# Kernel tuning notes

Measured on AMD Instinct MI355X. Metric: run time of the kernel, lower is better.

The kernel has to match this reference:

```python
import jax, jax.numpy as jnp
import numpy as np

B, H, W, C = 8, 64, 64, 128
BN_EPS = 1e-3  # keras BatchNormalization default epsilon


def setup_inputs() -> dict:
    key = jax.random.key(0)
    ks = jax.random.split(key, 8)
    scale = 1.0 / np.sqrt(C)
    return {
        "x": jax.random.normal(ks[0], (B, H, W, C), dtype=jnp.float32),
        "wq": jax.random.normal(ks[1], (C, C), dtype=jnp.float32) * scale,
        "bq": jnp.zeros((C,), dtype=jnp.float32),
        "wk": jax.random.normal(ks[2], (C, C), dtype=jnp.float32) * scale,
        "bk": jnp.zeros((C,), dtype=jnp.float32),
        "wv": jax.random.normal(ks[3], (C, C), dtype=jnp.float32) * scale,
        "bv": jnp.zeros((C,), dtype=jnp.float32),
        "gamma": jnp.ones((C,), dtype=jnp.float32),
        "beta": jnp.zeros((C,), dtype=jnp.float32),
        "mov_mean": jax.random.normal(ks[4], (C,), dtype=jnp.float32) * 0.1,
        "mov_var": jax.random.uniform(ks[5], (C,), dtype=jnp.float32) * 0.5 + 0.5,
    }


def reference(x, wq, bq, wk, bk, wv, bv, gamma, beta, mov_mean, mov_var):
    b, h, w, c = x.shape
    n = h * w
    # 1x1 convs == per-pixel linear projections
    q = (jnp.einsum('bhwc,cd->bhwd', x, wq) + bq).reshape(b, n, c)
    k = (jnp.einsum('bhwc,cd->bhwd', x, wk) + bk).reshape(b, n, c)
    v = (jnp.einsum('bhwc,cd->bhwd', x, wv) + bv).reshape(b, n, c)
    # full [n, n] attention matrix (as in the original module)
    scores = jnp.einsum('bnc,bmc->bnm', q, k) / jnp.sqrt(jnp.asarray(c, x.dtype))
    attn = jax.nn.softmax(scores, axis=-1)  # dropout is identity in inference
    out = jnp.einsum('bnm,bmc->bnc', attn, v).reshape(b, h, w, c)
    out = out + x  # residual
    # BatchNormalization, inference mode (moving statistics)
    inv = gamma * jax.lax.rsqrt(mov_var + BN_EPS)
    out = out * inv + (beta - mov_mean * inv)
    return out
```

## Files before the change

kernel.cpp:

```cpp
#include <hip/hip_runtime.h>


typedef __attribute__((ext_vector_type(8))) short bf16x8;
typedef __attribute__((ext_vector_type(4))) float f32x4;

__device__ __forceinline__ unsigned short f2bf(float f) {
  unsigned int u = __builtin_bit_cast(unsigned int, f);
  u += 0x7fffu + ((u >> 16) & 1u);
  return (unsigned short)(u >> 16);
}
__device__ __forceinline__ unsigned int pack2(float a, float b) {
  return (unsigned int)f2bf(a) | ((unsigned int)f2bf(b) << 16);
}
__device__ __forceinline__ unsigned int pack2t(float a, float b) {
  return __builtin_amdgcn_perm(__builtin_bit_cast(unsigned int, b),
                               __builtin_bit_cast(unsigned int, a),
                               0x07060302u);
}
__device__ __forceinline__ float fexp2(float x) {
  return __builtin_amdgcn_exp2f(x);
}

__device__ __forceinline__ void dma16(const void* g, void* l) {
  __builtin_amdgcn_global_load_lds(
      (const __attribute__((address_space(1))) unsigned int*)g,
      (__attribute__((address_space(3))) unsigned int*)l, 16, 0, 0);
}

#define SCALE_Q (0.08838834764831845f * 1.44269504088896340f)

__global__ __launch_bounds__(256) void prep_wt(
    const float* __restrict__ wq, const float* __restrict__ wk,
    const float* __restrict__ wv, unsigned short* __restrict__ wt) {
  __shared__ float ws[128 * 129];
  const float* W = (blockIdx.x == 0) ? wq : (blockIdx.x == 1 ? wk : wv);
  const float sc = (blockIdx.x == 0) ? SCALE_Q : 1.0f;
  unsigned short* out = wt + blockIdx.x * 16384;
  const int t = threadIdx.x;

#pragma unroll
  for (int i = 0; i < 16; ++i) {
    int e = (i * 256 + t) * 4;
    float4 v = *(const float4*)(W + e);
    int k = e >> 7, c = e & 127;
    float* d = ws + k * 129 + c;
    d[0] = v.x; d[1] = v.y; d[2] = v.z; d[3] = v.w;
  }
  __syncthreads();

  const int c = t & 15, n0 = t >> 4;
#pragma unroll
  for (int pass = 0; pass < 8; ++pass) {
    int n = pass * 16 + n0;
    const float* col = ws + n;
    unsigned int u0 = pack2(col[(c * 8 + 0) * 129] * sc, col[(c * 8 + 1) * 129] * sc);
    unsigned int u1 = pack2(col[(c * 8 + 2) * 129] * sc, col[(c * 8 + 3) * 129] * sc);
    unsigned int u2 = pack2(col[(c * 8 + 4) * 129] * sc, col[(c * 8 + 5) * 129] * sc);
    unsigned int u3 = pack2(col[(c * 8 + 6) * 129] * sc, col[(c * 8 + 7) * 129] * sc);
    *(uint4*)(out + n * 128 + c * 8) = make_uint4(u0, u1, u2, u3);
  }
}

__global__ __launch_bounds__(256) void qkv_proj(
    const float* __restrict__ x, const unsigned short* __restrict__ wt,
    const float* __restrict__ bq, const float* __restrict__ bk, const float* __restrict__ bv,
    unsigned short* __restrict__ Qg, unsigned short* __restrict__ Kg,
    unsigned short* __restrict__ Vtg) {
  __shared__ unsigned short xs[64 * 128];
  __shared__ unsigned short obuf[9216];
  const int t = threadIdx.x;
  const int rowblk = blockIdx.x * 64;

#pragma unroll
  for (int i = 0; i < 8; ++i) {
    int flat = t * 4 + i * 1024;
    int row = flat >> 7, col = flat & 127;
    float4 v = *(const float4*)(x + (size_t)(rowblk + row) * 128 + col);
    unsigned int u0 = pack2(v.x, v.y), u1 = pack2(v.z, v.w);
    int pos = (col >> 3) ^ (row & 15);
    *(uint2*)(xs + row * 128 + pos * 8 + (col & 7)) = make_uint2(u0, u1);
  }
  __syncthreads();

  const int lane = t & 63, wv_ = t >> 6;
  const int lm = lane & 15, quad = lane >> 4;

  bf16x8 a[4];
  {
    int row = wv_ * 16 + lm;
#pragma unroll
    for (int ks = 0; ks < 4; ++ks)
      a[ks] = __builtin_bit_cast(bf16x8,
          *(const uint4*)(xs + row * 128 + (((ks * 4 + quad) ^ lm) * 8)));
  }

  const int b   = rowblk >> 12;
  const int nb0 = rowblk & 4095;
  const f32x4 zero4 = {0.f, 0.f, 0.f, 0.f};

#pragma unroll
  for (int p = 0; p < 3; ++p) {
    const unsigned short* w = wt + p * 16384;
    const float* bias = (p == 0) ? bq : (p == 1 ? bk : bv);
    const float bsc = (p == 0) ? SCALE_Q : 1.0f;

    f32x4 acc[8];
#pragma unroll
    for (int ct = 0; ct < 8; ++ct) acc[ct] = zero4;

#pragma unroll
    for (int ct = 0; ct < 8; ++ct) {
      int n = ct * 16 + lm;
      const uint4* wp = (const uint4*)(w + n * 128 + quad * 8);
#pragma unroll
      for (int ks = 0; ks < 4; ++ks) {
        bf16x8 bfr = __builtin_bit_cast(bf16x8, wp[ks * 4]);
        acc[ct] = __builtin_amdgcn_mfma_f32_16x16x32_bf16(a[ks], bfr, acc[ct], 0, 0, 0);
      }
    }

    if (p < 2) {
      int rowb = wv_ * 16 + quad * 4;
#pragma unroll
      for (int ct = 0; ct < 8; ++ct) {
        int c = ct * 16 + lm;
        float bb = bias[c] * bsc;
#pragma unroll
        for (int r = 0; r < 4; ++r)
          obuf[(rowb + r) * 136 + c] = f2bf(acc[ct][r] + bb);
      }
      __syncthreads();
      unsigned short* og = (p == 0) ? Qg : Kg;
      int row = t >> 2;
#pragma unroll
      for (int j = 0; j < 4; ++j) {
        int pos = (t & 3) * 4 + j;
        int ch  = (p == 1) ? (pos ^ (row & 15)) : pos;
        uint4 vv = *(const uint4*)(obuf + row * 136 + ch * 8);
        *(uint4*)(og + (size_t)(rowblk + row) * 128 + pos * 8) = vv;
      }
      __syncthreads();
    } else {
      int key_base = wv_ * 16 + quad * 4;
#pragma unroll
      for (int ct = 0; ct < 8; ++ct) {
        int c = ct * 16 + lm;
        float bb = bias[c];
        unsigned int u0 = pack2(acc[ct][0] + bb, acc[ct][1] + bb);
        unsigned int u1 = pack2(acc[ct][2] + bb, acc[ct][3] + bb);
        *(uint2*)(obuf + c * 72 + key_base) = make_uint2(u0, u1);
      }
      __syncthreads();
      int d = t >> 1;
#pragma unroll
      for (int j = 0; j < 4; ++j) {
        int ch = (t & 1) * 4 + j;
        uint4 vv = *(const uint4*)(obuf + d * 72 + ch * 8);
        *(uint4*)(Vtg + (size_t)b * 524288 + (size_t)d * 4096 + nb0 + ch * 8) = vv;
      }
    }
  }
}

__global__ __launch_bounds__(256)
__attribute__((amdgpu_waves_per_eu(2, 2)))
void flash_attn(
    const unsigned short* __restrict__ Qg, const unsigned short* __restrict__ Kg,
    const unsigned short* __restrict__ Vtg, const float* __restrict__ x,
    const float* __restrict__ gamma, const float* __restrict__ beta,
    const float* __restrict__ mmean, const float* __restrict__ mvar,
    float* __restrict__ out) {
  __shared__ unsigned short Kt[16384];
  __shared__ unsigned short Pbuf[2][8192];

  const int b  = blockIdx.x & 7;
  const int qt = blockIdx.x >> 3;
  const int t = threadIdx.x;
  const int lane = t & 63;
  const int w = t >> 6;
  const int lm = lane & 15, quad = lane >> 4;
  const int q0 = qt * 64;

  const unsigned short* Qb = Qg  + (size_t)b * 524288;
  const unsigned short* Kb = Kg  + (size_t)b * 524288;
  const unsigned short* Vb = Vtg + (size_t)b * 524288;

  {
    const unsigned short* src = Kb + (size_t)w * 4096 + lane * 8;
    unsigned short* dst = &Kt[w * 4096];
#pragma unroll
    for (int j = 0; j < 8; ++j) dma16(src + j * 512, dst + j * 512);
  }

  bf16x8 qf[4][4];
#pragma unroll
  for (int nt = 0; nt < 4; ++nt) {
    const uint4* qp = (const uint4*)(Qb + (size_t)(q0 + nt * 16 + lm) * 128 + quad * 8);
#pragma unroll
    for (int ks = 0; ks < 4; ++ks) qf[nt][ks] = __builtin_bit_cast(bf16x8, qp[ks * 4]);
  }

  const f32x4 zero4 = {0.f, 0.f, 0.f, 0.f};
  f32x4 o[2][4];
#pragma unroll
  for (int mt = 0; mt < 2; ++mt)
#pragma unroll
    for (int nt = 0; nt < 4; ++nt) o[mt][nt] = zero4;
  float lp[4] = {0.f, 0.f, 0.f, 0.f};
  bf16x8 vf[2][4];

#pragma unroll 1
  for (int kt = 0; kt < 32; ++kt) {
    const int key0 = kt * 128;

    asm volatile("s_waitcnt vmcnt(8)" ::: "memory");

    f32x4 sa[2][4];
#pragma unroll
    for (int mt = 0; mt < 2; ++mt)
#pragma unroll
      for (int nt = 0; nt < 4; ++nt) sa[mt][nt] = zero4;
#pragma unroll
    for (int mt = 0; mt < 2; ++mt) {
      const unsigned short* kr = &Kt[(w * 32 + mt * 16 + lm) * 128];
      bf16x8 kf[4];
#pragma unroll
      for (int ks = 0; ks < 4; ++ks)
        kf[ks] = __builtin_bit_cast(bf16x8, *(const uint4*)(kr + ((ks * 4 + quad) ^ lm) * 8));
#pragma unroll
      for (int ks = 0; ks < 4; ++ks)
#pragma unroll
        for (int nt = 0; nt < 4; ++nt)
          sa[mt][nt] = __builtin_amdgcn_mfma_f32_16x16x32_bf16(kf[ks], qf[nt][ks], sa[mt][nt], 0, 0, 0);
    }

    asm volatile("s_waitcnt lgkmcnt(0)" ::: "memory");
    if (kt + 1 < 32) {
      const unsigned short* src = Kb + (size_t)(kt + 1) * 16384 + w * 4096 + lane * 8;
      unsigned short* dst = &Kt[w * 4096];
#pragma unroll
      for (int j = 0; j < 8; ++j) dma16(src + j * 512, dst + j * 512);
    }

    if (kt > 0) {
      const uint4* Pr = (const uint4*)Pbuf[(kt & 1) ^ 1];
#pragma unroll
      for (int nt = 0; nt < 4; ++nt) {
        bf16x8 pf[4];
#pragma unroll
        for (int ks = 0; ks < 4; ++ks)
          pf[ks] = __builtin_bit_cast(bf16x8, Pr[(nt * 16 + lm) * 16 + ((ks * 4 + quad) ^ lm)]);
#pragma unroll
        for (int ks = 0; ks < 4; ++ks)
#pragma unroll
          for (int mt = 0; mt < 2; ++mt)
            o[mt][nt] = __builtin_amdgcn_mfma_f32_16x16x32_bf16(vf[mt][ks], pf[ks], o[mt][nt], 0, 0, 0);
      }
    }

#pragma unroll
    for (int mt = 0; mt < 2; ++mt) {
      const uint4* vp = (const uint4*)(Vb + (size_t)(w * 32 + mt * 16 + lm) * 4096 + key0 + quad * 8);
#pragma unroll
      for (int ks = 0; ks < 4; ++ks) vf[mt][ks] = __builtin_bit_cast(bf16x8, vp[ks * 4]);
    }

    {
      unsigned short* Ps = Pbuf[kt & 1];
      const int sub = (quad & 1) * 4;
#pragma unroll
      for (int mt = 0; mt < 2; ++mt) {
        int c16 = w * 4 + mt * 2 + (quad >> 1);
        int pos = c16 ^ lm;
#pragma unroll
        for (int nt = 0; nt < 4; ++nt) {
          float e0 = fexp2(sa[mt][nt][0]), e1 = fexp2(sa[mt][nt][1]);
          float e2 = fexp2(sa[mt][nt][2]), e3 = fexp2(sa[mt][nt][3]);
          lp[nt] += (e0 + e1) + (e2 + e3);
          *(uint2*)(Ps + (nt * 16 + lm) * 128 + pos * 8 + sub) =
              make_uint2(pack2t(e0, e1), pack2t(e2, e3));
        }
      }
    }

    asm volatile("s_waitcnt lgkmcnt(0)\n\ts_barrier" ::: "memory");
  }

  {
    const uint4* Pr = (const uint4*)Pbuf[1];
#pragma unroll
    for (int nt = 0; nt < 4; ++nt) {
      bf16x8 pf[4];
#pragma unroll
      for (int ks = 0; ks < 4; ++ks)
        pf[ks] = __builtin_bit_cast(bf16x8, Pr[(nt * 16 + lm) * 16 + ((ks * 4 + quad) ^ lm)]);
#pragma unroll
      for (int ks = 0; ks < 4; ++ks)
#pragma unroll
        for (int mt = 0; mt < 2; ++mt)
          o[mt][nt] = __builtin_amdgcn_mfma_f32_16x16x32_bf16(vf[mt][ks], pf[ks], o[mt][nt], 0, 0, 0);
    }
  }

  float* lred = (float*)Pbuf[0];
#pragma unroll
  for (int nt = 0; nt < 4; ++nt) {
    lp[nt] += __shfl_xor(lp[nt], 16);
    lp[nt] += __shfl_xor(lp[nt], 32);
  }
  if (quad == 0) {
#pragma unroll
    for (int nt = 0; nt < 4; ++nt) lred[w * 64 + nt * 16 + lm] = lp[nt];
  }
  __syncthreads();
  float rl[4];
#pragma unroll
  for (int nt = 0; nt < 4; ++nt) {
    int q = nt * 16 + lm;
    rl[nt] = 1.0f / ((lred[q] + lred[64 + q]) + (lred[128 + q] + lred[192 + q]));
  }

#pragma unroll
  for (int mt = 0; mt < 2; ++mt) {
    int c0 = w * 32 + mt * 16 + quad * 4;
    float4 gm = *(const float4*)(gamma + c0);
    float4 bt = *(const float4*)(beta + c0);
    float4 mm = *(const float4*)(mmean + c0);
    float4 mv = *(const float4*)(mvar + c0);
    float iv0 = gm.x * rsqrtf(mv.x + 1e-3f), iv1 = gm.y * rsqrtf(mv.y + 1e-3f);
    float iv2 = gm.z * rsqrtf(mv.z + 1e-3f), iv3 = gm.w * rsqrtf(mv.w + 1e-3f);
    float ad0 = bt.x - mm.x * iv0, ad1 = bt.y - mm.y * iv1;
    float ad2 = bt.z - mm.z * iv2, ad3 = bt.w - mm.w * iv3;
#pragma unroll
    for (int nt = 0; nt < 4; ++nt) {
      size_t g = ((size_t)b * 4096 + q0 + nt * 16 + lm) * 128 + c0;
      float4 xr = *(const float4*)(x + g);
      float4 ov;
      ov.x = (o[mt][nt][0] * rl[nt] + xr.x) * iv0 + ad0;
      ov.y = (o[mt][nt][1] * rl[nt] + xr.y) * iv1 + ad1;
      ov.z = (o[mt][nt][2] * rl[nt] + xr.z) * iv2 + ad2;
      ov.w = (o[mt][nt][3] * rl[nt] + xr.w) * iv3 + ad3;
      *(float4*)(out + g) = ov;
    }
  }
}

extern "C" void kernel_launch(void* const* d_in, const int* in_sizes, int n_in,
                              void* d_out, int out_size, void* d_ws, size_t ws_size,
                              hipStream_t stream) {
  const float* x     = (const float*)d_in[0];
  const float* wq    = (const float*)d_in[1];
  const float* bq    = (const float*)d_in[2];
  const float* wk    = (const float*)d_in[3];
  const float* bk    = (const float*)d_in[4];
  const float* wv    = (const float*)d_in[5];
  const float* bv    = (const float*)d_in[6];
  const float* gamma = (const float*)d_in[7];
  const float* beta  = (const float*)d_in[8];
  const float* mmean = (const float*)d_in[9];
  const float* mvar  = (const float*)d_in[10];
  float* out = (float*)d_out;

  unsigned short* wt  = (unsigned short*)d_ws;
  unsigned short* Qg  = wt + 3 * 128 * 128;
  unsigned short* Kg  = Qg + 8 * 4096 * 128;
  unsigned short* Vtg = Kg + 8 * 4096 * 128;

  prep_wt<<<dim3(3), dim3(256), 0, stream>>>(wq, wk, wv, wt);
  qkv_proj<<<dim3(512), dim3(256), 0, stream>>>(x, wt, bq, bk, bv, Qg, Kg, Vtg);
  flash_attn<<<dim3(512), dim3(256), 0, stream>>>(Qg, Kg, Vtg, x, gamma, beta,
                                                  mmean, mvar, out);
}
```

Baseline: 208.1 us.

## Split attention block across eight waves and drop P double-buffering

The attention kernel now launches 512 threads per block. Key/channel work is split across four wave groups and queries across two, so each wave holds half the query fragments and accumulators. The P double buffer and the one-iteration software pipeline (PV of the previous tile overlapped with QK of the current) are replaced by a single P buffer. This requires a second barrier per key tile, and V is now loaded at the top of each iteration. The aim is more waves per CU and lower register pressure to hide latency, at the cost of more synchronisation and less explicit overlap.

```diff
diff --git a/kernel.cpp b/kernel.cpp
--- a/kernel.cpp
+++ b/kernel.cpp
@@ -162,8 +162,8 @@
   }
 }
 
-__global__ __launch_bounds__(256)
-__attribute__((amdgpu_waves_per_eu(2, 2)))
+__global__ __launch_bounds__(512)
+__attribute__((amdgpu_waves_per_eu(4, 4)))
 void flash_attn(
     const unsigned short* __restrict__ Qg, const unsigned short* __restrict__ Kg,
     const unsigned short* __restrict__ Vtg, const float* __restrict__ x,
@@ -171,13 +171,14 @@
     const float* __restrict__ mmean, const float* __restrict__ mvar,
     float* __restrict__ out) {
   __shared__ unsigned short Kt[16384];
-  __shared__ unsigned short Pbuf[2][8192];
+  __shared__ unsigned short Pbuf[8192];
 
   const int b  = blockIdx.x & 7;
   const int qt = blockIdx.x >> 3;
   const int t = threadIdx.x;
   const int lane = t & 63;
   const int w = t >> 6;
+  const int kw = w >> 1, qw = w & 1;
   const int lm = lane & 15, quad = lane >> 4;
   const int q0 = qt * 64;
 
@@ -186,43 +187,51 @@
   const unsigned short* Vb = Vtg + (size_t)b * 524288;
 
   {
-    const unsigned short* src = Kb + (size_t)w * 4096 + lane * 8;
-    unsigned short* dst = &Kt[w * 4096];
-#pragma unroll
-    for (int j = 0; j < 8; ++j) dma16(src + j * 512, dst + j * 512);
-  }
-
-  bf16x8 qf[4][4];
-#pragma unroll
-  for (int nt = 0; nt < 4; ++nt) {
-    const uint4* qp = (const uint4*)(Qb + (size_t)(q0 + nt * 16 + lm) * 128 + quad * 8);
+    const unsigned short* src = Kb + (size_t)w * 2048 + lane * 8;
+    unsigned short* dst = &Kt[w * 2048];
+#pragma unroll
+    for (int j = 0; j < 4; ++j) dma16(src + j * 512, dst + j * 512);
+  }
+
+  bf16x8 qf[2][4];
+#pragma unroll
+  for (int nt = 0; nt < 2; ++nt) {
+    const uint4* qp = (const uint4*)(Qb + (size_t)(q0 + qw * 32 + nt * 16 + lm) * 128 + quad * 8);
 #pragma unroll
     for (int ks = 0; ks < 4; ++ks) qf[nt][ks] = __builtin_bit_cast(bf16x8, qp[ks * 4]);
   }
 
+  asm volatile("s_waitcnt vmcnt(8)" ::: "memory");
+  __builtin_amdgcn_s_barrier();
+
   const f32x4 zero4 = {0.f, 0.f, 0.f, 0.f};
-  f32x4 o[2][4];
+  f32x4 o[2][2];
 #pragma unroll
   for (int mt = 0; mt < 2; ++mt)
 #pragma unroll
-    for (int nt = 0; nt < 4; ++nt) o[mt][nt] = zero4;
-  float lp[4] = {0.f, 0.f, 0.f, 0.f};
-  bf16x8 vf[2][4];
+    for (int nt = 0; nt < 2; ++nt) o[mt][nt] = zero4;
+  float lp[2] = {0.f, 0.f};
 
 #pragma unroll 1
   for (int kt = 0; kt < 32; ++kt) {
     const int key0 = kt * 128;
 
-    asm volatile("s_waitcnt vmcnt(8)" ::: "memory");
-
-    f32x4 sa[2][4];
+    bf16x8 vf[2][4];
+#pragma unroll
+    for (int mt = 0; mt < 2; ++mt) {
+      const uint4* vp = (const uint4*)(Vb + (size_t)(kw * 32 + mt * 16 + lm) * 4096 + key0 + quad * 8);
+#pragma unroll
+      for (int ks = 0; ks < 4; ++ks) vf[mt][ks] = __builtin_bit_cast(bf16x8, vp[ks * 4]);
+    }
+
+    f32x4 sa[2][2];
 #pragma unroll
     for (int mt = 0; mt < 2; ++mt)
 #pragma unroll
-      for (int nt = 0; nt < 4; ++nt) sa[mt][nt] = zero4;
+      for (int nt = 0; nt < 2; ++nt) sa[mt][nt] = zero4;
 #pragma unroll
     for (int mt = 0; mt < 2; ++mt) {
-      const unsigned short* kr = &Kt[(w * 32 + mt * 16 + lm) * 128];
+      const unsigned short* kr = &Kt[(kw * 32 + mt * 16 + lm) * 128];
       bf16x8 kf[4];
 #pragma unroll
       for (int ks = 0; ks < 4; ++ks)
@@ -230,99 +239,77 @@
 #pragma unroll
       for (int ks = 0; ks < 4; ++ks)
 #pragma unroll
-        for (int nt = 0; nt < 4; ++nt)
+        for (int nt = 0; nt < 2; ++nt)
           sa[mt][nt] = __builtin_amdgcn_mfma_f32_16x16x32_bf16(kf[ks], qf[nt][ks], sa[mt][nt], 0, 0, 0);
     }
 
-    asm volatile("s_waitcnt lgkmcnt(0)" ::: "memory");
-    if (kt + 1 < 32) {
-      const unsigned short* src = Kb + (size_t)(kt + 1) * 16384 + w * 4096 + lane * 8;
-      unsigned short* dst = &Kt[w * 4096];
-#pragma unroll
-      for (int j = 0; j < 8; ++j) dma16(src + j * 512, dst + j * 512);
-    }
-
-    if (kt > 0) {
-      const uint4* Pr = (const uint4*)Pbuf[(kt & 1) ^ 1];
-#pragma unroll
-      for (int nt = 0; nt < 4; ++nt) {
-        bf16x8 pf[4];
-#pragma unroll
-        for (int ks = 0; ks < 4; ++ks)
-          pf[ks] = __builtin_bit_cast(bf16x8, Pr[(nt * 16 + lm) * 16 + ((ks * 4 + quad) ^ lm)]);
-#pragma unroll
-        for (int ks = 0; ks < 4; ++ks)
-#pragma unroll
-          for (int mt = 0; mt < 2; ++mt)
-            o[mt][nt] = __builtin_amdgcn_mfma_f32_16x16x32_bf16(vf[mt][ks], pf[ks], o[mt][nt], 0, 0, 0);
-      }
-    }
-
-#pragma unroll
-    for (int mt = 0; mt < 2; ++mt) {
-      const uint4* vp = (const uint4*)(Vb + (size_t)(w * 32 + mt * 16 + lm) * 4096 + key0 + quad * 8);
-#pragma unroll
-      for (int ks = 0; ks < 4; ++ks) vf[mt][ks] = __builtin_bit_cast(bf16x8, vp[ks * 4]);
-    }
-
     {
-      unsigned short* Ps = Pbuf[kt & 1];
       const int sub = (quad & 1) * 4;
 #pragma unroll
       for (int mt = 0; mt < 2; ++mt) {
-        int c16 = w * 4 + mt * 2 + (quad >> 1);
+        int c16 = kw * 4 + mt * 2 + (quad >> 1);
         int pos = c16 ^ lm;
 #pragma unroll
-        for (int nt = 0; nt < 4; ++nt) {
+        for (int nt = 0; nt < 2; ++nt) {
           float e0 = fexp2(sa[mt][nt][0]), e1 = fexp2(sa[mt][nt][1]);
           float e2 = fexp2(sa[mt][nt][2]), e3 = fexp2(sa[mt][nt][3]);
           lp[nt] += (e0 + e1) + (e2 + e3);
-          *(uint2*)(Ps + (nt * 16 + lm) * 128 + pos * 8 + sub) =
+          *(uint2*)(Pbuf + (qw * 32 + nt * 16 + lm) * 128 + pos * 8 + sub) =
               make_uint2(pack2t(e0, e1), pack2t(e2, e3));
         }
       }
     }
 
     asm volatile("s_waitcnt lgkmcnt(0)\n\ts_barrier" ::: "memory");
-  }
-
-  {
-    const uint4* Pr = (const uint4*)Pbuf[1];
-#pragma unroll
-    for (int nt = 0; nt < 4; ++nt) {
-      bf16x8 pf[4];
-#pragma unroll
-      for (int ks = 0; ks < 4; ++ks)
-        pf[ks] = __builtin_bit_cast(bf16x8, Pr[(nt * 16 + lm) * 16 + ((ks * 4 + quad) ^ lm)]);
-#pragma unroll
-      for (int ks = 0; ks < 4; ++ks)
-#pragma unroll
-        for (int mt = 0; mt < 2; ++mt)
-          o[mt][nt] = __builtin_amdgcn_mfma_f32_16x16x32_bf16(vf[mt][ks], pf[ks], o[mt][nt], 0, 0, 0);
-    }
-  }
-
-  float* lred = (float*)Pbuf[0];
-#pragma unroll
-  for (int nt = 0; nt < 4; ++nt) {
+
+    if (kt + 1 < 32) {
+      const unsigned short* src = Kb + (size_t)(kt + 1) * 16384 + w * 2048 + lane * 8;
+      unsigned short* dst = &Kt[w * 2048];
+#pragma unroll
+      for (int j = 0; j < 4; ++j) dma16(src + j * 512, dst + j * 512);
+    }
+
+    {
+      const uint4* Pr = (const uint4*)Pbuf;
+#pragma unroll
+      for (int nt = 0; nt < 2; ++nt) {
+        bf16x8 pf[4];
+#pragma unroll
+        for (int ks = 0; ks < 4; ++ks)
+          pf[ks] = __builtin_bit_cast(bf16x8, Pr[(qw * 32 + nt * 16 + lm) * 16 + ((ks * 4 + quad) ^ lm)]);
+#pragma unroll
+        for (int ks = 0; ks < 4; ++ks)
+#pragma unroll
+          for (int mt = 0; mt < 2; ++mt)
+            o[mt][nt] = __builtin_amdgcn_mfma_f32_16x16x32_bf16(vf[mt][ks], pf[ks], o[mt][nt], 0, 0, 0);
+      }
+    }
+
+    asm volatile("s_waitcnt vmcnt(0) lgkmcnt(0)\n\ts_barrier" ::: "memory");
+  }
+
+  float* lred = (float*)Pbuf;
+#pragma unroll
+  for (int nt = 0; nt < 2; ++nt) {
     lp[nt] += __shfl_xor(lp[nt], 16);
     lp[nt] += __shfl_xor(lp[nt], 32);
   }
   if (quad == 0) {
 #pragma unroll
-    for (int nt = 0; nt < 4; ++nt) lred[w * 64 + nt * 16 + lm] = lp[nt];
+    for (int nt = 0; nt < 2; ++nt)
+      lred[kw * 64 + qw * 32 + nt * 16 + lm] = lp[nt];
   }
   __syncthreads();
-  float rl[4];
-#pragma unroll
-  for (int nt = 0; nt < 4; ++nt) {
-    int q = nt * 16 + lm;
+  float rl[2];
+#pragma unroll
+  for (int nt = 0; nt < 2; ++nt) {
+    int q = qw * 32 + nt * 16 + lm;
     rl[nt] = 1.0f / ((lred[q] + lred[64 + q]) + (lred[128 + q] + lred[192 + q]));
   }
 
 #pragma unroll
   for (int mt = 0; mt < 2; ++mt) {
-    int c0 = w * 32 + mt * 16 + quad * 4;
+    int c0 = kw * 32 + mt * 16 + quad * 4;
     float4 gm = *(const float4*)(gamma + c0);
     float4 bt = *(const float4*)(beta + c0);
     float4 mm = *(const float4*)(mmean + c0);
@@ -332,8 +319,8 @@
     float ad0 = bt.x - mm.x * iv0, ad1 = bt.y - mm.y * iv1;
     float ad2 = bt.z - mm.z * iv2, ad3 = bt.w - mm.w * iv3;
 #pragma unroll
-    for (int nt = 0; nt < 4; ++nt) {
-      size_t g = ((size_t)b * 4096 + q0 + nt * 16 + lm) * 128 + c0;
+    for (int nt = 0; nt < 2; ++nt) {
+      size_t g = ((size_t)b * 4096 + q0 + qw * 32 + nt * 16 + lm) * 128 + c0;
       float4 xr = *(const float4*)(x + g);
       float4 ov;
       ov.x = (o[mt][nt][0] * rl[nt] + xr.x) * iv0 + ad0;
@@ -368,6 +355,6 @@
 
   prep_wt<<<dim3(3), dim3(256), 0, stream>>>(wq, wk, wv, wt);
   qkv_proj<<<dim3(512), dim3(256), 0, stream>>>(x, wt, bq, bk, bv, Qg, Kg, Vtg);
-  flash_attn<<<dim3(512), dim3(256), 0, stream>>>(Qg, Kg, Vtg, x, gamma, beta,
+  flash_attn<<<dim3(512), dim3(512), 0, stream>>>(Qg, Kg, Vtg, x, gamma, beta,
                                                   mmean, mvar, out);
 }
```

New measurement: 273.9 us. +31.6%, slower.

## Software-pipeline softmax exp of previous tile behind current QK MFMAs

Applied to the files above, without the earlier changes.

Restructures the flash attention key loop into a two-phase macro that keeps two score register sets. The exp/pack/store of the previous tile's scores is deferred so it can overlap with the current tile's QK^T MFMAs, and the PV product now follows a single barrier. The goal is to hide the exp and LDS write latency behind matrix work. The cost is an extra 32 accumulator registers, which risks spills under the two-waves-per-EU bound, plus a reworked epilogue for the last tile.

```diff
diff --git a/kernel.cpp b/kernel.cpp
--- a/kernel.cpp
+++ b/kernel.cpp
@@ -161,6 +161,75 @@
     }
   }
 }
+
+
+#define PHASE(KT, SAC, SAP)                                                    \
+  {                                                                            \
+    const int kt_ = (KT);                                                      \
+        \
+    asm volatile("s_waitcnt vmcnt(8)" ::: "memory");                           \
+    _Pragma("unroll") for (int mt = 0; mt < 2; ++mt)                           \
+      _Pragma("unroll") for (int nt = 0; nt < 4; ++nt) SAC[mt][nt] = zero4;    \
+    _Pragma("unroll") for (int mt = 0; mt < 2; ++mt) {                         \
+      const unsigned short* kr = &Kt[(w * 32 + mt * 16 + lm) * 128];           \
+      bf16x8 kf[4];                                                            \
+      _Pragma("unroll") for (int ks = 0; ks < 4; ++ks)                         \
+        kf[ks] = __builtin_bit_cast(                                           \
+            bf16x8, *(const uint4*)(kr + ((ks * 4 + quad) ^ lm) * 8));         \
+      _Pragma("unroll") for (int ks = 0; ks < 4; ++ks)                         \
+        _Pragma("unroll") for (int nt = 0; nt < 4; ++nt)                       \
+          SAC[mt][nt] = __builtin_amdgcn_mfma_f32_16x16x32_bf16(               \
+              kf[ks], qf[nt][ks], SAC[mt][nt], 0, 0, 0);                       \
+    }                                                                          \
+        \
+    if (kt_ > 0) {                                                             \
+      unsigned short* Ps = Pbuf[(kt_ - 1) & 1];                                \
+      const int sub = (quad & 1) * 4;                                          \
+      _Pragma("unroll") for (int mt = 0; mt < 2; ++mt) {                       \
+        int c16 = w * 4 + mt * 2 + (quad >> 1);                                \
+        int pos = c16 ^ lm;                                                    \
+        _Pragma("unroll") for (int nt = 0; nt < 4; ++nt) {                     \
+          float e0 = fexp2(SAP[mt][nt][0]), e1 = fexp2(SAP[mt][nt][1]);        \
+          float e2 = fexp2(SAP[mt][nt][2]), e3 = fexp2(SAP[mt][nt][3]);        \
+          lp[nt] += (e0 + e1) + (e2 + e3);                                     \
+          *(uint2*)(Ps + (nt * 16 + lm) * 128 + pos * 8 + sub) =               \
+              make_uint2(pack2t(e0, e1), pack2t(e2, e3));                      \
+        }                                                                      \
+      }                                                                        \
+    }                                                                          \
+       \
+    asm volatile("s_waitcnt lgkmcnt(0)" ::: "memory");                         \
+    if (kt_ + 1 < 32) {                                                        \
+      const unsigned short* src =                                              \
+          Kb + (size_t)(kt_ + 1) * 16384 + w * 4096 + lane * 8;                \
+      unsigned short* dst = &Kt[w * 4096];                                     \
+      _Pragma("unroll") for (int j = 0; j < 8; ++j)                            \
+        dma16(src + j * 512, dst + j * 512);                                   \
+    }                                                                          \
+              \
+    asm volatile("s_barrier" ::: "memory");                                    \
+                \
+    if (kt_ > 0) {                                                             \
+      const uint4* Pr = (const uint4*)Pbuf[(kt_ - 1) & 1];                     \
+      _Pragma("unroll") for (int nt = 0; nt < 4; ++nt) {                       \
+        bf16x8 pf[4];                                                          \
+        _Pragma("unroll") for (int ks = 0; ks < 4; ++ks)                       \
+          pf[ks] = __builtin_bit_cast(                                         \
+              bf16x8, Pr[(nt * 16 + lm) * 16 + ((ks * 4 + quad) ^ lm)]);       \
+        _Pragma("unroll") for (int ks = 0; ks < 4; ++ks)                       \
+          _Pragma("unroll") for (int mt = 0; mt < 2; ++mt)                     \
+            o[mt][nt] = __builtin_amdgcn_mfma_f32_16x16x32_bf16(               \
+                vf[mt][ks], pf[ks], o[mt][nt], 0, 0, 0);                       \
+      }                                                                        \
+    }                                                                          \
+                      \
+    _Pragma("unroll") for (int mt = 0; mt < 2; ++mt) {                         \
+      const uint4* vp = (const uint4*)(                                        \
+          Vb + (size_t)(w * 32 + mt * 16 + lm) * 4096 + kt_ * 128 + quad * 8); \
+      _Pragma("unroll") for (int ks = 0; ks < 4; ++ks)                         \
+        vf[mt][ks] = __builtin_bit_cast(bf16x8, vp[ks * 4]);                   \
+    }                                                                          \
+  }
 
 __global__ __launch_bounds__(256)
 __attribute__((amdgpu_waves_per_eu(2, 2)))
@@ -208,83 +277,32 @@
     for (int nt = 0; nt < 4; ++nt) o[mt][nt] = zero4;
   float lp[4] = {0.f, 0.f, 0.f, 0.f};
   bf16x8 vf[2][4];
+  f32x4 saA[2][4], saB[2][4];
 
 #pragma unroll 1
-  for (int kt = 0; kt < 32; ++kt) {
-    const int key0 = kt * 128;
-
-    asm volatile("s_waitcnt vmcnt(8)" ::: "memory");
-
-    f32x4 sa[2][4];
-#pragma unroll
-    for (int mt = 0; mt < 2; ++mt)
-#pragma unroll
-      for (int nt = 0; nt < 4; ++nt) sa[mt][nt] = zero4;
+  for (int kt2 = 0; kt2 < 16; ++kt2) {
+    PHASE(2 * kt2,     saA, saB)
+    PHASE(2 * kt2 + 1, saB, saA)
+  }
+
+  {
+    unsigned short* Ps = Pbuf[1];
+    const int sub = (quad & 1) * 4;
 #pragma unroll
     for (int mt = 0; mt < 2; ++mt) {
-      const unsigned short* kr = &Kt[(w * 32 + mt * 16 + lm) * 128];
-      bf16x8 kf[4];
-#pragma unroll
-      for (int ks = 0; ks < 4; ++ks)
-        kf[ks] = __builtin_bit_cast(bf16x8, *(const uint4*)(kr + ((ks * 4 + quad) ^ lm) * 8));
-#pragma unroll
-      for (int ks = 0; ks < 4; ++ks)
-#pragma unroll
-        for (int nt = 0; nt < 4; ++nt)
-          sa[mt][nt] = __builtin_amdgcn_mfma_f32_16x16x32_bf16(kf[ks], qf[nt][ks], sa[mt][nt], 0, 0, 0);
-    }
-
-    asm volatile("s_waitcnt lgkmcnt(0)" ::: "memory");
-    if (kt + 1 < 32) {
-      const unsigned short* src = Kb + (size_t)(kt + 1) * 16384 + w * 4096 + lane * 8;
-      unsigned short* dst = &Kt[w * 4096];
-#pragma unroll
-      for (int j = 0; j < 8; ++j) dma16(src + j * 512, dst + j * 512);
-    }
-
-    if (kt > 0) {
-      const uint4* Pr = (const uint4*)Pbuf[(kt & 1) ^ 1];
+      int c16 = w * 4 + mt * 2 + (quad >> 1);
+      int pos = c16 ^ lm;
 #pragma unroll
       for (int nt = 0; nt < 4; ++nt) {
-        bf16x8 pf[4];
-#pragma unroll
-        for (int ks = 0; ks < 4; ++ks)
-          pf[ks] = __builtin_bit_cast(bf16x8, Pr[(nt * 16 + lm) * 16 + ((ks * 4 + quad) ^ lm)]);
-#pragma unroll
-        for (int ks = 0; ks < 4; ++ks)
-#pragma unroll
-          for (int mt = 0; mt < 2; ++mt)
-            o[mt][nt] = __builtin_amdgcn_mfma_f32_16x16x32_bf16(vf[mt][ks], pf[ks], o[mt][nt], 0, 0, 0);
-      }
-    }
-
-#pragma unroll
-    for (int mt = 0; mt < 2; ++mt) {
-      const uint4* vp = (const uint4*)(Vb + (size_t)(w * 32 + mt * 16 + lm) * 4096 + key0 + quad * 8);
-#pragma unroll
-      for (int ks = 0; ks < 4; ++ks) vf[mt][ks] = __builtin_bit_cast(bf16x8, vp[ks * 4]);
-    }
-
-    {
-      unsigned short* Ps = Pbuf[kt & 1];
-      const int sub = (quad & 1) * 4;
-#pragma unroll
-      for (int mt = 0; mt < 2; ++mt) {
-        int c16 = w * 4 + mt * 2 + (quad >> 1);
-        int pos = c16 ^ lm;
-#pragma unroll
-        for (int nt = 0; nt < 4; ++nt) {
-          float e0 = fexp2(sa[mt][nt][0]), e1 = fexp2(sa[mt][nt][1]);
-          float e2 = fexp2(sa[mt][nt][2]), e3 = fexp2(sa[mt][nt][3]);
-          lp[nt] += (e0 + e1) + (e2 + e3);
-          *(uint2*)(Ps + (nt * 16 + lm) * 128 + pos * 8 + sub) =
-              make_uint2(pack2t(e0, e1), pack2t(e2, e3));
-        }
-      }
-    }
-
-    asm volatile("s_waitcnt lgkmcnt(0)\n\ts_barrier" ::: "memory");
-  }
+        float e0 = fexp2(saB[mt][nt][0]), e1 = fexp2(saB[mt][nt][1]);
+        float e2 = fexp2(saB[mt][nt][2]), e3 = fexp2(saB[mt][nt][3]);
+        lp[nt] += (e0 + e1) + (e2 + e3);
+        *(uint2*)(Ps + (nt * 16 + lm) * 128 + pos * 8 + sub) =
+            make_uint2(pack2t(e0, e1), pack2t(e2, e3));
+      }
+    }
+  }
+  asm volatile("s_waitcnt lgkmcnt(0)\n\ts_barrier" ::: "memory");
 
   {
     const uint4* Pr = (const uint4*)Pbuf[1];
```

New measurement: 209.4 us. No clear change (+0.6%).
